# Optimization experiments

Hardware: AMD Instinct MI355X
Metric: run time of the kernel (lower is better)

The kernel has to match this reference:

```python
import jax, jax.numpy as jnp
import numpy as np

D = 1024
DFF = 4096  # SwiGLU hidden = 4*d_model
EPS = 1e-6

def rmsnorm(x, w):
    return x * jax.lax.rsqrt(jnp.mean(x * x, axis=-1, keepdims=True) + EPS) * w

def mingru_scan(gates, cands):
    # h_t = g_t * h_{t-1} + (1 - g_t) * c_t, h_0 = 0 -> linear recurrence,
    # solved with an associative scan over pairs (a, b): h = a*h_prev + b.
    a = gates
    b = (1.0 - gates) * cands
    def combine(e1, e2):
        a1, b1 = e1
        a2, b2 = e2
        return (a1 * a2, a2 * b1 + b2)
    _, h = jax.lax.associative_scan(combine, (a, b), axis=1)
    return h

def setup_inputs() -> dict:
    key = jax.random.key(0)
    ks = jax.random.split(key, 10)
    xavier = lambda k, fan_in, fan_out: jax.random.uniform(
        k, (fan_in, fan_out), jnp.float32,
        -np.sqrt(6.0 / (fan_in + fan_out)), np.sqrt(6.0 / (fan_in + fan_out)))
    return {
        "x": jax.random.normal(ks[0], (4, 4096, D), jnp.float32),
        "Wg": xavier(ks[1], D, D),
        "bg": jnp.ones((D,), jnp.float32),   # gate bias init = 1.0
        "Wc": xavier(ks[2], D, D),
        "bc": jnp.zeros((D,), jnp.float32),
        "n1_w": jnp.ones((D,), jnp.float32),
        "n2_w": jnp.ones((D,), jnp.float32),
        "W1": xavier(ks[3], D, DFF),   # SwiGLU gate proj
        "W3": xavier(ks[4], D, DFF),   # SwiGLU up proj
        "W2": xavier(ks[5], DFF, D),   # SwiGLU down proj
    }

def reference(x, Wg, bg, Wc, bc, n1_w, n2_w, W1, W3, W2):
    # --- MinGRU sub-block (pre-norm, residual) ---
    h_in = rmsnorm(x, n1_w)
    gates = jax.nn.sigmoid(jnp.einsum('bld,de->ble', h_in, Wg) + bg)
    cands = jnp.tanh(jnp.einsum('bld,de->ble', h_in, Wc) + bc)
    x = x + mingru_scan(gates, cands)
    # --- SwiGLU FFN sub-block (pre-norm, residual) ---
    f_in = rmsnorm(x, n2_w)
    ff = jnp.einsum('blf,fd->bld',
                    jax.nn.silu(jnp.einsum('bld,df->blf', f_in, W1))
                    * jnp.einsum('bld,df->blf', f_in, W3), W2)
    return x + ff
```

## Files before the change

kernel.cpp:

```cpp
#include <hip/hip_runtime.h>
#include <hip/hip_bf16.h>
#include <math.h>

typedef __bf16 bf16_t;
typedef bf16_t bf16x8 __attribute__((ext_vector_type(8)));
typedef bf16_t bf16x4 __attribute__((ext_vector_type(4)));
typedef bf16_t bf16x2 __attribute__((ext_vector_type(2)));
typedef float f32x4 __attribute__((ext_vector_type(4)));

#define D_MODEL 1024
#define SEQ     4096
#define BATCH   4
#define NTOK    16384
#define DFF     4096
#define CLEN    64
#define NCHUNK  64
#define NCH     4096

__device__ __forceinline__ void gload16(const bf16_t* g, bf16_t* l) {
    __builtin_amdgcn_global_load_lds(
        (const __attribute__((address_space(1))) void*)g,
        (__attribute__((address_space(3))) void*)l, 16, 0, 0);
}

__global__ void transpose_to_bf16(const float* __restrict__ W,
                                  bf16_t* __restrict__ Wt, int R, int C) {
    __shared__ float tile[32][33];
    const int c0 = blockIdx.x * 32, r0 = blockIdx.y * 32;
    const int tx = threadIdx.x, ty = threadIdx.y;
#pragma unroll
    for (int j = 0; j < 32; j += 8)
        tile[ty + j][tx] = W[(size_t)(r0 + ty + j) * C + c0 + tx];
    __syncthreads();
#pragma unroll
    for (int j = 0; j < 32; j += 8)
        Wt[(size_t)(c0 + ty + j) * R + r0 + tx] = (bf16_t)tile[tx][ty + j];
}

__global__ void rmsnorm_kernel(const float* __restrict__ x,
                               const float* __restrict__ w,
                               bf16_t* __restrict__ out) {
    const int row = blockIdx.x;
    const int tid = threadIdx.x;
    const float4 v = ((const float4*)(x + (size_t)row * D_MODEL))[tid];
    float ss = v.x * v.x + v.y * v.y + v.z * v.z + v.w * v.w;
#pragma unroll
    for (int o = 1; o < 64; o <<= 1) ss += __shfl_xor(ss, o);
    __shared__ float red[4];
    if ((tid & 63) == 0) red[tid >> 6] = ss;
    __syncthreads();
    const float tot = red[0] + red[1] + red[2] + red[3];
    const float scale = rsqrtf(tot * (1.0f / D_MODEL) + 1e-6f);
    const float4 wv = ((const float4*)w)[tid];
    bf16x4 o4;
    o4[0] = (bf16_t)(v.x * scale * wv.x);
    o4[1] = (bf16_t)(v.y * scale * wv.y);
    o4[2] = (bf16_t)(v.z * scale * wv.z);
    o4[3] = (bf16_t)(v.w * scale * wv.w);
    ((bf16x4*)(out + (size_t)row * D_MODEL))[tid] = o4;
}

#define MFMA16(a, b, c) __builtin_amdgcn_mfma_f32_16x16x32_bf16((a), (b), (c), 0, 0, 0)

template <int MODE>
__global__ __launch_bounds__(512, 2)
void gemm8p(const bf16_t* __restrict__ A, const bf16_t* __restrict__ B1t,
            const bf16_t* __restrict__ B2t, const float* __restrict__ bias1,
            const float* __restrict__ bias2, bf16x2* __restrict__ GC,
            bf16_t* __restrict__ Ot, float* __restrict__ O,
            int N, int K, int lg_nbn) {
    constexpr bool DUAL = (MODE != 2);
    constexpr int BN = DUAL ? 128 : 256;
    constexpr int NFR = DUAL ? 2 : 4;
    __shared__ bf16_t lds[65536];

    const int tid = threadIdx.x;
    const int lane = tid & 63;
    const int wave = tid >> 6;
    const int wr = wave >> 2, wc = wave & 3;
    const int lr16 = lane & 15, lk = lane >> 4;

    const int nwg = gridDim.x;
    const int wg = blockIdx.x;
    const int swg = (wg & 7) * (nwg >> 3) + (wg >> 3);
    const int bn = swg & ((1 << lg_nbn) - 1);
    const int bm = swg >> lg_nbn;
    const int nt = K >> 6;

    const int lr8 = lane >> 3;
    const int cge = ((lane & 7) ^ lr8) << 3;
    const bf16_t* Ag  = A   + (size_t)(bm * 256 + wave * 8 + lr8) * K + cge;
    const bf16_t* B1g = B1t + (size_t)(bn * BN  + wave * 8 + lr8) * K + cge;
    const bf16_t* B2g = DUAL ? (B2t + (size_t)(bn * BN + wave * 8 + lr8) * K + cge)
                             : (const bf16_t*)nullptr;

    f32x4 acc1[8][NFR] = {};
    f32x4 acc2[DUAL ? 8 : 1][NFR] = {};

    auto stageA = [&](int u) {
        bf16_t* dst = &lds[(u & 1) * 32768 + wave * 512];
        const bf16_t* src = Ag + ((size_t)u << 6);
        gload16(src,                     dst);
        gload16(src + ((size_t)64  * K), dst + 4096);
        gload16(src + ((size_t)128 * K), dst + 8192);
        gload16(src + ((size_t)192 * K), dst + 12288);
    };
    auto stageB = [&](int u) {
        bf16_t* dst = &lds[(u & 1) * 32768 + 16384 + wave * 512];
        const bf16_t* src = B1g + ((size_t)u << 6);
        gload16(src,                    dst);
        gload16(src + ((size_t)64 * K), dst + 4096);
        if constexpr (DUAL) {
            bf16_t* dst2 = &lds[(u & 1) * 32768 + 24576 + wave * 512];
            const bf16_t* src2 = B2g + ((size_t)u << 6);
            gload16(src2,                    dst2);
            gload16(src2 + ((size_t)64 * K), dst2 + 4096);
        } else {
            gload16(src + ((size_t)128 * K), dst + 8192);
            gload16(src + ((size_t)192 * K), dst + 12288);
        }
    };
    auto rdA = [&](int p, int m, int ks) {
        const int row = wr * 128 + m * 16 + lr16;
        const int c = ks * 4 + lk;
        return *(const bf16x8*)&lds[p * 32768 + row * 64 + (((c ^ row) & 7) << 3)];
    };
    auto rdB = [&](int p, int mat, int n, int ks) {
        const int row = wc * (BN / 4) + n * 16 + lr16;
        const int c = ks * 4 + lk;
        return *(const bf16x8*)&lds[p * 32768 + 16384 + mat * 8192 + row * 64 +
                                    (((c ^ row) & 7) << 3)];
    };

    stageA(0);
    stageB(0);
    asm volatile("s_waitcnt vmcnt(0)" ::: "memory");
    __builtin_amdgcn_s_barrier();

    for (int t = 0; t < nt; ++t) {
        const int p = t & 1;
        const bool pre = (t + 1 < nt);
        bf16x8 bF[DUAL ? 2 : 1][NFR];
        bf16x8 aF[4];

#pragma unroll
        for (int n = 0; n < NFR; ++n) {
            bF[0][n] = rdB(p, 0, n, 0);
            if constexpr (DUAL) bF[1][n] = rdB(p, 1, n, 0);
        }
#pragma unroll
        for (int m = 0; m < 4; ++m) aF[m] = rdA(p, m, 0);
        if (pre) stageA(t + 1);
        __builtin_amdgcn_s_barrier();
        asm volatile("s_waitcnt lgkmcnt(0)" ::: "memory");
        __builtin_amdgcn_sched_barrier(0);
        __builtin_amdgcn_s_setprio(1);
#pragma unroll
        for (int m = 0; m < 4; ++m)
#pragma unroll
            for (int n = 0; n < NFR; ++n) {
                acc1[m][n] = MFMA16(aF[m], bF[0][n], acc1[m][n]);
                if constexpr (DUAL) acc2[m][n] = MFMA16(aF[m], bF[1][n], acc2[m][n]);
            }
        __builtin_amdgcn_s_setprio(0);
        __builtin_amdgcn_s_barrier();

#pragma unroll
        for (int m = 0; m < 4; ++m) aF[m] = rdA(p, 4 + m, 0);
        if (pre) stageB(t + 1);
        __builtin_amdgcn_s_barrier();
        asm volatile("s_waitcnt lgkmcnt(0)" ::: "memory");
        __builtin_amdgcn_sched_barrier(0);
        __builtin_amdgcn_s_setprio(1);
#pragma unroll
        for (int m = 0; m < 4; ++m)
#pragma unroll
            for (int n = 0; n < NFR; ++n) {
                acc1[4 + m][n] = MFMA16(aF[m], bF[0][n], acc1[4 + m][n]);
                if constexpr (DUAL) acc2[4 + m][n] = MFMA16(aF[m], bF[1][n], acc2[4 + m][n]);
            }
        __builtin_amdgcn_s_setprio(0);
        __builtin_amdgcn_s_barrier();

#pragma unroll
        for (int n = 0; n < NFR; ++n) {
            bF[0][n] = rdB(p, 0, n, 1);
            if constexpr (DUAL) bF[1][n] = rdB(p, 1, n, 1);
        }
#pragma unroll
        for (int m = 0; m < 4; ++m) aF[m] = rdA(p, m, 1);
        __builtin_amdgcn_s_barrier();
        asm volatile("s_waitcnt lgkmcnt(0)" ::: "memory");
        __builtin_amdgcn_sched_barrier(0);
        __builtin_amdgcn_s_setprio(1);
#pragma unroll
        for (int m = 0; m < 4; ++m)
#pragma unroll
            for (int n = 0; n < NFR; ++n) {
                acc1[m][n] = MFMA16(aF[m], bF[0][n], acc1[m][n]);
                if constexpr (DUAL) acc2[m][n] = MFMA16(aF[m], bF[1][n], acc2[m][n]);
            }
        __builtin_amdgcn_s_setprio(0);
        __builtin_amdgcn_s_barrier();

#pragma unroll
        for (int m = 0; m < 4; ++m) aF[m] = rdA(p, 4 + m, 1);
        __builtin_amdgcn_s_barrier();
        asm volatile("s_waitcnt lgkmcnt(0)" ::: "memory");
        __builtin_amdgcn_sched_barrier(0);
        __builtin_amdgcn_s_setprio(1);
#pragma unroll
        for (int m = 0; m < 4; ++m)
#pragma unroll
            for (int n = 0; n < NFR; ++n) {
                acc1[4 + m][n] = MFMA16(aF[m], bF[0][n], acc1[4 + m][n]);
                if constexpr (DUAL) acc2[4 + m][n] = MFMA16(aF[m], bF[1][n], acc2[4 + m][n]);
            }
        __builtin_amdgcn_s_setprio(0);
        asm volatile("s_waitcnt vmcnt(0)" ::: "memory");
        __builtin_amdgcn_s_barrier();
    }

    const int rowBase = bm * 256 + wr * 128;
    const int colBase = bn * BN + wc * (BN / 4);
#pragma unroll
    for (int n = 0; n < NFR; ++n) {
        const int col = colBase + n * 16 + lr16;
        float b1v = 0.f, b2v = 0.f;
        if constexpr (MODE == 0) { b1v = bias1[col]; b2v = bias2[col]; }
#pragma unroll
        for (int m = 0; m < 8; ++m) {
#pragma unroll
            for (int j = 0; j < 4; ++j) {
                const int row = rowBase + m * 16 + lk * 4 + j;
                const size_t idx = (size_t)row * N + col;
                if constexpr (MODE == 0) {
                    const float gv = 1.0f / (1.0f + __expf(-(acc1[m][n][j] + b1v)));
                    const float cv = tanhf(acc2[m][n][j] + b2v);
                    bf16x2 pk;
                    pk[0] = (bf16_t)gv;
                    pk[1] = (bf16_t)cv;
                    GC[idx] = pk;
                } else if constexpr (MODE == 1) {
                    const float a = acc1[m][n][j];
                    const float s = a / (1.0f + __expf(-a));
                    Ot[idx] = (bf16_t)(s * acc2[m][n][j]);
                } else {
                    O[idx] += acc1[m][n][j];
                }
            }
        }
    }
}

__global__ void scan_phase1(const bf16x2* __restrict__ gc,
                            float* __restrict__ cA, float* __restrict__ cB) {
    const int d = blockIdx.x * 256 + threadIdx.x;
    const int b = blockIdx.y;
    const int cidx = blockIdx.z;
    const int ch = b * D_MODEL + d;
    const size_t base = ((size_t)b * SEQ + (size_t)cidx * CLEN) * D_MODEL + d;
    float A = 1.0f, Bv = 0.0f;
#pragma unroll 8
    for (int t = 0; t < CLEN; ++t) {
        const bf16x2 v = gc[base + (size_t)t * D_MODEL];
        const float gv = (float)v[0], cv = (float)v[1];
        Bv = gv * Bv + (1.0f - gv) * cv;
        A *= gv;
    }
    cA[cidx * NCH + ch] = A;
    cB[cidx * NCH + ch] = Bv;
}

__global__ void scan_phase2(const float* __restrict__ cA,
                            const float* __restrict__ cB,
                            float* __restrict__ hstart) {
    const int ch = blockIdx.x * 256 + threadIdx.x;
    float h = 0.0f;
#pragma unroll 8
    for (int cdx = 0; cdx < NCHUNK; ++cdx) {
        hstart[cdx * NCH + ch] = h;
        h = cA[cdx * NCH + ch] * h + cB[cdx * NCH + ch];
    }
}

__global__ void scan_phase3(const bf16x2* __restrict__ gc,
                            const float* __restrict__ hstart,
                            const float* __restrict__ x,
                            float* __restrict__ x1) {
    const int d = blockIdx.x * 256 + threadIdx.x;
    const int b = blockIdx.y;
    const int cidx = blockIdx.z;
    const int ch = b * D_MODEL + d;
    const size_t base = ((size_t)b * SEQ + (size_t)cidx * CLEN) * D_MODEL + d;
    float h = hstart[cidx * NCH + ch];
#pragma unroll 8
    for (int t = 0; t < CLEN; ++t) {
        const size_t off = base + (size_t)t * D_MODEL;
        const bf16x2 v = gc[off];
        const float gv = (float)v[0], cv = (float)v[1];
        h = gv * h + (1.0f - gv) * cv;
        x1[off] = x[off] + h;
    }
}

extern "C" void kernel_launch(void* const* d_in, const int* in_sizes, int n_in,
                              void* d_out, int out_size, void* d_ws,
                              size_t ws_size, hipStream_t stream) {
    const float* x   = (const float*)d_in[0];
    const float* Wg  = (const float*)d_in[1];
    const float* bg  = (const float*)d_in[2];
    const float* Wc  = (const float*)d_in[3];
    const float* bc  = (const float*)d_in[4];
    const float* n1w = (const float*)d_in[5];
    const float* n2w = (const float*)d_in[6];
    const float* W1  = (const float*)d_in[7];
    const float* W3  = (const float*)d_in[8];
    const float* W2  = (const float*)d_in[9];
    float* out = (float*)d_out;

    char* p = (char*)d_ws;
    bf16_t* tbuf  = (bf16_t*)p;
    bf16_t* h_in  = (bf16_t*)p;  p += (size_t)NTOK * D_MODEL * 2;
    bf16x2* gcbuf = (bf16x2*)p;  p += (size_t)NTOK * D_MODEL * 4;
    p += (size_t)32 << 20;
    bf16_t* f_in  = (bf16_t*)p;  p += (size_t)NTOK * D_MODEL * 2;
    bf16_t* Wg_t  = (bf16_t*)p;  p += (size_t)D_MODEL * D_MODEL * 2;
    bf16_t* Wc_t  = (bf16_t*)p;  p += (size_t)D_MODEL * D_MODEL * 2;
    bf16_t* W1_t  = (bf16_t*)p;  p += (size_t)DFF * D_MODEL * 2;
    bf16_t* W3_t  = (bf16_t*)p;  p += (size_t)DFF * D_MODEL * 2;
    bf16_t* W2_t  = (bf16_t*)p;  p += (size_t)D_MODEL * DFF * 2;
    float* cA     = (float*)p;   p += (size_t)NCHUNK * NCH * 4;
    float* cB     = (float*)p;   p += (size_t)NCHUNK * NCH * 4;
    float* hstart = (float*)p;   p += (size_t)NCHUNK * NCH * 4;

    const dim3 tb(32, 8);
    transpose_to_bf16<<<dim3(1024 / 32, 1024 / 32), tb, 0, stream>>>(Wg, Wg_t, 1024, 1024);
    transpose_to_bf16<<<dim3(1024 / 32, 1024 / 32), tb, 0, stream>>>(Wc, Wc_t, 1024, 1024);
    transpose_to_bf16<<<dim3(4096 / 32, 1024 / 32), tb, 0, stream>>>(W1, W1_t, 1024, 4096);
    transpose_to_bf16<<<dim3(4096 / 32, 1024 / 32), tb, 0, stream>>>(W3, W3_t, 1024, 4096);
    transpose_to_bf16<<<dim3(1024 / 32, 4096 / 32), tb, 0, stream>>>(W2, W2_t, 4096, 1024);

    rmsnorm_kernel<<<NTOK, 256, 0, stream>>>(x, n1w, h_in);

    gemm8p<0><<<512, 512, 0, stream>>>(h_in, Wg_t, Wc_t, bg, bc, gcbuf,
                                       nullptr, nullptr, D_MODEL, D_MODEL, 3);

    scan_phase1<<<dim3(D_MODEL / 256, BATCH, NCHUNK), 256, 0, stream>>>(gcbuf, cA, cB);
    scan_phase2<<<NCH / 256, 256, 0, stream>>>(cA, cB, hstart);
    scan_phase3<<<dim3(D_MODEL / 256, BATCH, NCHUNK), 256, 0, stream>>>(gcbuf, hstart, x, out);

    rmsnorm_kernel<<<NTOK, 256, 0, stream>>>(out, n2w, f_in);

    gemm8p<1><<<2048, 512, 0, stream>>>(f_in, W1_t, W3_t, nullptr, nullptr,
                                        nullptr, tbuf, nullptr, DFF, D_MODEL, 5);

    gemm8p<2><<<256, 512, 0, stream>>>(tbuf, W2_t, nullptr, nullptr, nullptr,
                                       nullptr, nullptr, out, D_MODEL, DFF, 2);
}
```

Baseline: 765.1 us.

## Register double-buffer GEMM fragments and fuse scan phase3 with RMSNorm

Restructures the GEMM main loop to prefetch the next k-slice's LDS fragments into registers while MFMAs run, replacing many per-substep barriers and priority hints with one sync per tile. Also fuses the final scan phase with the second RMSNorm, so the residual output is normalized in the same kernel without re-reading it. The fused kernel uses far fewer blocks with a per-timestep block sync, which can reduce parallelism. Register pressure in the GEMM rises from holding two fragment sets.

```diff
diff --git a/kernel.cpp b/kernel.cpp
--- a/kernel.cpp
+++ b/kernel.cpp
@@ -72,6 +72,7 @@
     constexpr bool DUAL = (MODE != 2);
     constexpr int BN = DUAL ? 128 : 256;
     constexpr int NFR = DUAL ? 2 : 4;
+    constexpr int NMAT = DUAL ? 2 : 1;
     __shared__ bf16_t lds[65536];
 
     const int tid = threadIdx.x;
@@ -132,93 +133,77 @@
                                     (((c ^ row) & 7) << 3)];
     };
 
+    bf16x8 aFc[4], aFn[4];
+    bf16x8 bF0[NMAT][NFR], bF1[NMAT][NFR];
+
     stageA(0);
     stageB(0);
-    asm volatile("s_waitcnt vmcnt(0)" ::: "memory");
-    __builtin_amdgcn_s_barrier();
+    __syncthreads();
+#pragma unroll
+    for (int m = 0; m < 4; ++m) aFc[m] = rdA(0, m, 0);
+#pragma unroll
+    for (int mat = 0; mat < NMAT; ++mat)
+#pragma unroll
+        for (int n = 0; n < NFR; ++n) bF0[mat][n] = rdB(0, mat, n, 0);
 
     for (int t = 0; t < nt; ++t) {
         const int p = t & 1;
         const bool pre = (t + 1 < nt);
-        bf16x8 bF[DUAL ? 2 : 1][NFR];
-        bf16x8 aF[4];
-
-#pragma unroll
-        for (int n = 0; n < NFR; ++n) {
-            bF[0][n] = rdB(p, 0, n, 0);
-            if constexpr (DUAL) bF[1][n] = rdB(p, 1, n, 0);
+
+#pragma unroll
+        for (int m = 0; m < 4; ++m) aFn[m] = rdA(p, 4 + m, 0);
+#pragma unroll
+        for (int mat = 0; mat < NMAT; ++mat)
+#pragma unroll
+            for (int n = 0; n < NFR; ++n) bF1[mat][n] = rdB(p, mat, n, 1);
+        if (pre) stageA(t + 1);
+#pragma unroll
+        for (int m = 0; m < 4; ++m)
+#pragma unroll
+            for (int n = 0; n < NFR; ++n) {
+                acc1[m][n] = MFMA16(aFc[m], bF0[0][n], acc1[m][n]);
+                if constexpr (DUAL) acc2[m][n] = MFMA16(aFc[m], bF0[1][n], acc2[m][n]);
+            }
+
+#pragma unroll
+        for (int m = 0; m < 4; ++m) aFc[m] = rdA(p, m, 1);
+        if (pre) stageB(t + 1);
+#pragma unroll
+        for (int m = 0; m < 4; ++m)
+#pragma unroll
+            for (int n = 0; n < NFR; ++n) {
+                acc1[4 + m][n] = MFMA16(aFn[m], bF0[0][n], acc1[4 + m][n]);
+                if constexpr (DUAL) acc2[4 + m][n] = MFMA16(aFn[m], bF0[1][n], acc2[4 + m][n]);
+            }
+
+#pragma unroll
+        for (int m = 0; m < 4; ++m) aFn[m] = rdA(p, 4 + m, 1);
+#pragma unroll
+        for (int m = 0; m < 4; ++m)
+#pragma unroll
+            for (int n = 0; n < NFR; ++n) {
+                acc1[m][n] = MFMA16(aFc[m], bF1[0][n], acc1[m][n]);
+                if constexpr (DUAL) acc2[m][n] = MFMA16(aFc[m], bF1[1][n], acc2[m][n]);
+            }
+
+#pragma unroll
+        for (int m = 0; m < 4; ++m)
+#pragma unroll
+            for (int n = 0; n < NFR; ++n) {
+                acc1[4 + m][n] = MFMA16(aFn[m], bF1[0][n], acc1[4 + m][n]);
+                if constexpr (DUAL) acc2[4 + m][n] = MFMA16(aFn[m], bF1[1][n], acc2[4 + m][n]);
+            }
+
+        __syncthreads();
+        if (pre) {
+            const int q = p ^ 1;
+#pragma unroll
+            for (int m = 0; m < 4; ++m) aFc[m] = rdA(q, m, 0);
+#pragma unroll
+            for (int mat = 0; mat < NMAT; ++mat)
+#pragma unroll
+                for (int n = 0; n < NFR; ++n) bF0[mat][n] = rdB(q, mat, n, 0);
         }
-#pragma unroll
-        for (int m = 0; m < 4; ++m) aF[m] = rdA(p, m, 0);
-        if (pre) stageA(t + 1);
-        __builtin_amdgcn_s_barrier();
-        asm volatile("s_waitcnt lgkmcnt(0)" ::: "memory");
-        __builtin_amdgcn_sched_barrier(0);
-        __builtin_amdgcn_s_setprio(1);
-#pragma unroll
-        for (int m = 0; m < 4; ++m)
-#pragma unroll
-            for (int n = 0; n < NFR; ++n) {
-                acc1[m][n] = MFMA16(aF[m], bF[0][n], acc1[m][n]);
-                if constexpr (DUAL) acc2[m][n] = MFMA16(aF[m], bF[1][n], acc2[m][n]);
-            }
-        __builtin_amdgcn_s_setprio(0);
-        __builtin_amdgcn_s_barrier();
-
-#pragma unroll
-        for (int m = 0; m < 4; ++m) aF[m] = rdA(p, 4 + m, 0);
-        if (pre) stageB(t + 1);
-        __builtin_amdgcn_s_barrier();
-        asm volatile("s_waitcnt lgkmcnt(0)" ::: "memory");
-        __builtin_amdgcn_sched_barrier(0);
-        __builtin_amdgcn_s_setprio(1);
-#pragma unroll
-        for (int m = 0; m < 4; ++m)
-#pragma unroll
-            for (int n = 0; n < NFR; ++n) {
-                acc1[4 + m][n] = MFMA16(aF[m], bF[0][n], acc1[4 + m][n]);
-                if constexpr (DUAL) acc2[4 + m][n] = MFMA16(aF[m], bF[1][n], acc2[4 + m][n]);
-            }
-        __builtin_amdgcn_s_setprio(0);
-        __builtin_amdgcn_s_barrier();
-
-#pragma unroll
-        for (int n = 0; n < NFR; ++n) {
-            bF[0][n] = rdB(p, 0, n, 1);
-            if constexpr (DUAL) bF[1][n] = rdB(p, 1, n, 1);
-        }
-#pragma unroll
-        for (int m = 0; m < 4; ++m) aF[m] = rdA(p, m, 1);
-        __builtin_amdgcn_s_barrier();
-        asm volatile("s_waitcnt lgkmcnt(0)" ::: "memory");
-        __builtin_amdgcn_sched_barrier(0);
-        __builtin_amdgcn_s_setprio(1);
-#pragma unroll
-        for (int m = 0; m < 4; ++m)
-#pragma unroll
-            for (int n = 0; n < NFR; ++n) {
-                acc1[m][n] = MFMA16(aF[m], bF[0][n], acc1[m][n]);
-                if constexpr (DUAL) acc2[m][n] = MFMA16(aF[m], bF[1][n], acc2[m][n]);
-            }
-        __builtin_amdgcn_s_setprio(0);
-        __builtin_amdgcn_s_barrier();
-
-#pragma unroll
-        for (int m = 0; m < 4; ++m) aF[m] = rdA(p, 4 + m, 1);
-        __builtin_amdgcn_s_barrier();
-        asm volatile("s_waitcnt lgkmcnt(0)" ::: "memory");
-        __builtin_amdgcn_sched_barrier(0);
-        __builtin_amdgcn_s_setprio(1);
-#pragma unroll
-        for (int m = 0; m < 4; ++m)
-#pragma unroll
-            for (int n = 0; n < NFR; ++n) {
-                acc1[4 + m][n] = MFMA16(aF[m], bF[0][n], acc1[4 + m][n]);
-                if constexpr (DUAL) acc2[4 + m][n] = MFMA16(aF[m], bF[1][n], acc2[4 + m][n]);
-            }
-        __builtin_amdgcn_s_setprio(0);
-        asm volatile("s_waitcnt vmcnt(0)" ::: "memory");
-        __builtin_amdgcn_s_barrier();
     }
 
     const int rowBase = bm * 256 + wr * 128;
@@ -284,23 +269,47 @@
     }
 }
 
-__global__ void scan_phase3(const bf16x2* __restrict__ gc,
-                            const float* __restrict__ hstart,
-                            const float* __restrict__ x,
-                            float* __restrict__ x1) {
-    const int d = blockIdx.x * 256 + threadIdx.x;
+__global__ __launch_bounds__(256)
+void scan_phase3_norm(const bf16x2* __restrict__ gc,
+                      const float* __restrict__ hstart,
+                      const float* __restrict__ x,
+                      const float* __restrict__ n2w,
+                      float* __restrict__ x1out, bf16_t* __restrict__ f_in) {
+    const int tid = threadIdx.x;
+    const int cidx = blockIdx.x;
     const int b = blockIdx.y;
-    const int cidx = blockIdx.z;
-    const int ch = b * D_MODEL + d;
-    const size_t base = ((size_t)b * SEQ + (size_t)cidx * CLEN) * D_MODEL + d;
-    float h = hstart[cidx * NCH + ch];
-#pragma unroll 8
-    for (int t = 0; t < CLEN; ++t) {
-        const size_t off = base + (size_t)t * D_MODEL;
-        const bf16x2 v = gc[off];
-        const float gv = (float)v[0], cv = (float)v[1];
-        h = gv * h + (1.0f - gv) * cv;
-        x1[off] = x[off] + h;
+    const int d0 = tid * 4;
+    const float4 h4 = *(const float4*)&hstart[cidx * NCH + b * D_MODEL + d0];
+    float h0 = h4.x, h1 = h4.y, h2 = h4.z, h3 = h4.w;
+    const float4 w4 = *(const float4*)&n2w[d0];
+    __shared__ float red[2][4];
+    const size_t rowBase = (size_t)b * SEQ + (size_t)cidx * CLEN;
+    for (int tt = 0; tt < CLEN; ++tt) {
+        const size_t roff = (rowBase + tt) * D_MODEL + d0;
+        const bf16x8 gv = *(const bf16x8*)&gc[roff];
+        const float4 xv = *(const float4*)&x[roff];
+        float g, c, v0, v1, v2, v3;
+        g = (float)gv[0]; c = (float)gv[1]; h0 = g * h0 + (1.f - g) * c; v0 = xv.x + h0;
+        g = (float)gv[2]; c = (float)gv[3]; h1 = g * h1 + (1.f - g) * c; v1 = xv.y + h1;
+        g = (float)gv[4]; c = (float)gv[5]; h2 = g * h2 + (1.f - g) * c; v2 = xv.z + h2;
+        g = (float)gv[6]; c = (float)gv[7]; h3 = g * h3 + (1.f - g) * c; v3 = xv.w + h3;
+        float ss = v0 * v0 + v1 * v1 + v2 * v2 + v3 * v3;
+#pragma unroll
+        for (int o = 1; o < 64; o <<= 1) ss += __shfl_xor(ss, o);
+        const int pb = tt & 1;
+        if ((tid & 63) == 0) red[pb][tid >> 6] = ss;
+        __syncthreads();
+        const float tot = red[pb][0] + red[pb][1] + red[pb][2] + red[pb][3];
+        const float scale = rsqrtf(tot * (1.0f / D_MODEL) + 1e-6f);
+        float4 ov;
+        ov.x = v0; ov.y = v1; ov.z = v2; ov.w = v3;
+        *(float4*)&x1out[roff] = ov;
+        bf16x4 o4;
+        o4[0] = (bf16_t)(v0 * scale * w4.x);
+        o4[1] = (bf16_t)(v1 * scale * w4.y);
+        o4[2] = (bf16_t)(v2 * scale * w4.z);
+        o4[3] = (bf16_t)(v3 * scale * w4.w);
+        *(bf16x4*)&f_in[roff] = o4;
     }
 }
 
@@ -348,9 +357,8 @@
 
     scan_phase1<<<dim3(D_MODEL / 256, BATCH, NCHUNK), 256, 0, stream>>>(gcbuf, cA, cB);
     scan_phase2<<<NCH / 256, 256, 0, stream>>>(cA, cB, hstart);
-    scan_phase3<<<dim3(D_MODEL / 256, BATCH, NCHUNK), 256, 0, stream>>>(gcbuf, hstart, x, out);
-
-    rmsnorm_kernel<<<NTOK, 256, 0, stream>>>(out, n2w, f_in);
+    scan_phase3_norm<<<dim3(NCHUNK, BATCH), 256, 0, stream>>>(gcbuf, hstart, x,
+                                                              n2w, out, f_in);
 
     gemm8p<1><<<2048, 512, 0, stream>>>(f_in, W1_t, W3_t, nullptr, nullptr,
                                         nullptr, tbuf, nullptr, DFF, D_MODEL, 5);
```

Result: slower. 797.5 us (+4.2%).
